# Kernel tuning notes

Hardware: AMD Instinct MI355X
Metric: run time of the kernel (lower is better)

## Reference

```python
import jax, jax.numpy as jnp
import numpy as np

N_NODES = 50000
N_EDGES = 800000
H = 64      # node_hidden_size
S = 16      # static_feature_size
EF = 16     # edge_feature_size
ATT_IN = 2 * H + 2 * S + EF   # 176
ATT_W = 2 * H + EF            # 144
UPD_IN = 2 * H                # 128
UPD_W = 2 * H                 # 128


def setup_inputs() -> dict:
    key = jax.random.key(0)
    ks = jax.random.split(key, 12)
    x = jax.random.normal(ks[0], (N_NODES, H), dtype=jnp.float32)
    x_s = jax.random.normal(ks[1], (N_NODES, S), dtype=jnp.float32)
    edge_index = jax.random.randint(ks[2], (2, N_EDGES), 0, N_NODES, dtype=jnp.int32)
    edge_features = jax.random.normal(ks[3], (N_EDGES, EF), dtype=jnp.float32)

    def lin(k, out_dim, in_dim):
        lim = 1.0 / np.sqrt(in_dim)
        kw, kb = jax.random.split(k)
        W = jax.random.uniform(kw, (out_dim, in_dim), minval=-lim, maxval=lim, dtype=jnp.float32)
        b = jax.random.uniform(kb, (out_dim,), minval=-lim, maxval=lim, dtype=jnp.float32)
        return W, b

    att_w1, att_b1 = lin(ks[4], ATT_W, ATT_IN)
    att_w2, att_b2 = lin(ks[5], 1, ATT_W)
    upd_w1, upd_b1 = lin(ks[6], UPD_W, UPD_IN)
    upd_w2, upd_b2 = lin(ks[7], H, UPD_W)

    return {
        "x": x, "x_s": x_s, "edge_index": edge_index, "edge_features": edge_features,
        "att_w1": att_w1, "att_b1": att_b1, "att_w2": att_w2, "att_b2": att_b2,
        "upd_w1": upd_w1, "upd_b1": upd_b1, "upd_w2": upd_w2, "upd_b2": upd_b2,
    }


def segment_softmax(scores, segment_ids, num_segments):
    max_scores = jax.ops.segment_max(scores, segment_ids, num_segments=num_segments)
    exp_scores = jnp.exp(scores - max_scores[segment_ids])
    sum_exp = jax.ops.segment_sum(exp_scores, segment_ids, num_segments=num_segments)
    return exp_scores / (sum_exp[segment_ids] + 1e-9)


def reference(x, x_s, edge_index, edge_features,
              att_w1, att_b1, att_w2, att_b2,
              upd_w1, upd_b1, upd_w2, upd_b2):
    num_nodes = x.shape[0]
    src, dst = edge_index[0], edge_index[1]

    # gather per-edge features: [E, 2H+2S+EF]
    att_in = jnp.concatenate(
        [x[src], x[dst], x_s[src], x_s[dst], edge_features], axis=-1)

    # attention MLP (depth=1, relu hidden), squeeze to [E]
    h = jax.nn.relu(att_in @ att_w1.T + att_b1)
    raw = (h @ att_w2.T + att_b2).squeeze(-1)
    raw = jax.nn.leaky_relu(raw)

    attn = segment_softmax(raw, dst, num_nodes)

    # weighted scatter-sum of source hidden feats -> [N, H]
    aggregated = jax.ops.segment_sum(x[src] * attn[:, None], dst, num_segments=num_nodes)

    upd_in = jnp.concatenate([x, aggregated], axis=-1)
    u = jax.nn.relu(upd_in @ upd_w1.T + upd_b1)
    out = u @ upd_w2.T + upd_b2
    return jax.nn.relu(out)
```

## Files before the change

### kernel.cpp

```cpp
#include <hip/hip_runtime.h>
#include <math.h>

#define N_NODES_C 50000
#define E_C       800000
#define ATT_IN_C  176
#define ATT_HID_C 144
#define SCAN_B    98
#define UPD_TILES 3125
#define DEG_B     3125
#define CVT_B     1978
#define SCORE_B   256

typedef __attribute__((ext_vector_type(8))) __bf16 bf16x8;
typedef __attribute__((ext_vector_type(4))) float f32x4;

#define O_RAW   0L
#define O_DEG   3200000L
#define O_OFF   3400704L
#define O_CUR   3601408L
#define O_CSR   3802112L
#define O_EFC   7002112L
#define O_XB    32602112L
#define O_XSB   39002112L
#define O_W1B   40602112L
#define O_UW1B  40653312L
#define O_UW2B  40686080L
#define O_AGGB  40702464L
#define O_PSUM  O_AGGB

__device__ __forceinline__ bf16x8 bzero8() {
    bf16x8 z;
#pragma unroll
    for (int i = 0; i < 8; ++i) z[i] = (__bf16)0.0f;
    return z;
}

__global__ __launch_bounds__(256) void k_prep(
    const int* __restrict__ ei,
    const float* __restrict__ x, const float* __restrict__ xs,
    const float* __restrict__ w1,
    const float* __restrict__ uw1, const float* __restrict__ uw2,
    int* __restrict__ deg,
    __bf16* __restrict__ xb, __bf16* __restrict__ xsb,
    __bf16* __restrict__ w1b,
    __bf16* __restrict__ uw1b, __bf16* __restrict__ uw2b)
{
    int bid = blockIdx.x;
    if (bid < DEG_B) {
        int e = bid * 256 + threadIdx.x;
        if (e < E_C) atomicAdd(&deg[ei[E_C + e]], 1);
        return;
    }
    long g = (long)(bid - DEG_B) * 256 + threadIdx.x;
    const long G_X = 400000, G_XS = 500000, G_W1 = 503168,
               G_UW1 = 505216, G_UW2 = 506240;
    if (g >= G_UW2) return;
    const float* src; __bf16* dst; long off;
    if (g < G_X)        { src = x;   dst = xb;   off = g * 8; }
    else if (g < G_XS)  { src = xs;  dst = xsb;  off = (g - G_X) * 8; }
    else if (g < G_W1)  { src = w1;  dst = w1b;  off = (g - G_XS) * 8; }
    else if (g < G_UW1) { src = uw1; dst = uw1b; off = (g - G_W1) * 8; }
    else                { src = uw2; dst = uw2b; off = (g - G_UW1) * 8; }
    float4 a = *(const float4*)(src + off);
    float4 b = *(const float4*)(src + off + 4);
    bf16x8 o;
    o[0] = (__bf16)a.x; o[1] = (__bf16)a.y; o[2] = (__bf16)a.z; o[3] = (__bf16)a.w;
    o[4] = (__bf16)b.x; o[5] = (__bf16)b.y; o[6] = (__bf16)b.z; o[7] = (__bf16)b.w;
    *(bf16x8*)(dst + off) = o;
}

__global__ __launch_bounds__(256) void k_scan1(const int* __restrict__ deg,
                                               int* __restrict__ psum) {
    __shared__ int red[256];
    int b = blockIdx.x, t = threadIdx.x;
    int i = b * 512 + t * 2;
    int s = 0;
    if (i < N_NODES_C) s += deg[i];
    if (i + 1 < N_NODES_C) s += deg[i + 1];
    red[t] = s;
    __syncthreads();
#pragma unroll
    for (int off = 128; off > 0; off >>= 1) {
        if (t < off) red[t] += red[t + off];
        __syncthreads();
    }
    if (t == 0) psum[b] = red[0];
}

__global__ __launch_bounds__(256) void k_scan3(const int* __restrict__ deg,
                                               const int* __restrict__ psum,
                                               int* __restrict__ offsets,
                                               int* __restrict__ cursor) {
    __shared__ int sc[256];
    __shared__ int bo[2];
    int b = blockIdx.x, t = threadIdx.x;
    if (t < 64) {
        int v1 = (t < SCAN_B) ? psum[t] : 0;
        int v2 = (t + 64 < SCAN_B) ? psum[t + 64] : 0;
        int c   = ((t < b) ? v1 : 0) + ((t + 64 < b) ? v2 : 0);
        int tot = v1 + v2;
#pragma unroll
        for (int off = 32; off > 0; off >>= 1) {
            c   += __shfl_xor(c, off, 64);
            tot += __shfl_xor(tot, off, 64);
        }
        if (t == 0) { bo[0] = c; bo[1] = tot; }
    }
    int i = b * 512 + t * 2;
    int d0 = (i < N_NODES_C) ? deg[i] : 0;
    int d1 = (i + 1 < N_NODES_C) ? deg[i + 1] : 0;
    int s = d0 + d1;
    sc[t] = s;
    __syncthreads();
#pragma unroll
    for (int off = 1; off < 256; off <<= 1) {
        int val = sc[t];
        int add = (t >= off) ? sc[t - off] : 0;
        __syncthreads();
        sc[t] = val + add;
        __syncthreads();
    }
    int excl = bo[0] + sc[t] - s;
    if (i < N_NODES_C)     { offsets[i]     = excl;      cursor[i]     = excl; }
    if (i + 1 < N_NODES_C) { offsets[i + 1] = excl + d0; cursor[i + 1] = excl + d0; }
    if (b == 0 && t == 0)  offsets[N_NODES_C] = bo[1];
}

__global__ __launch_bounds__(256) void k_fill(const int* __restrict__ ei,
                                              const float* __restrict__ ef,
                                              int* __restrict__ cursor,
                                              unsigned* __restrict__ csrp,
                                              __bf16* __restrict__ efc) {
    int e = blockIdx.x * blockDim.x + threadIdx.x;
    if (e < E_C) {
        int src  = ei[e];
        int dst  = ei[E_C + e];
        int slot = atomicAdd(&cursor[dst], 1);
        csrp[slot] = (unsigned)src | ((unsigned)dst << 16);
        const float4* efp = (const float4*)(ef + (long)e * 16);
        float4 f0 = efp[0], f1 = efp[1], f2 = efp[2], f3 = efp[3];
        bf16x8 o0, o1;
        o0[0] = (__bf16)f0.x; o0[1] = (__bf16)f0.y; o0[2] = (__bf16)f0.z; o0[3] = (__bf16)f0.w;
        o0[4] = (__bf16)f1.x; o0[5] = (__bf16)f1.y; o0[6] = (__bf16)f1.z; o0[7] = (__bf16)f1.w;
        o1[0] = (__bf16)f2.x; o1[1] = (__bf16)f2.y; o1[2] = (__bf16)f2.z; o1[3] = (__bf16)f2.w;
        o1[4] = (__bf16)f3.x; o1[5] = (__bf16)f3.y; o1[6] = (__bf16)f3.z; o1[7] = (__bf16)f3.w;
        __bf16* d = efc + (long)slot * 16;
        *(bf16x8*)d       = o0;
        *(bf16x8*)(d + 8) = o1;
    }
}

__device__ __forceinline__ void load_afrags(
    int src, int dst, long slot, int quad,
    const __bf16* __restrict__ xb, const __bf16* __restrict__ xsb,
    const __bf16* __restrict__ efc,
    bf16x8 a[6])
{
    const __bf16* px = xb + (long)src * 64 + quad * 8;
    const __bf16* pd = xb + (long)dst * 64 + quad * 8;
    a[0] = *(const bf16x8*)(px);
    a[1] = *(const bf16x8*)(px + 32);
    a[2] = *(const bf16x8*)(pd);
    a[3] = *(const bf16x8*)(pd + 32);
    if (quad < 2) {
        a[4] = *(const bf16x8*)(xsb + (long)src * 16 + quad * 8);
        a[5] = *(const bf16x8*)(efc + slot * 16 + quad * 8);
    } else {
        a[4] = *(const bf16x8*)(xsb + (long)dst * 16 + (quad - 2) * 8);
        a[5] = bzero8();
    }
}

__global__ __launch_bounds__(256) void k_scores_mfma(
    const __bf16* __restrict__ xb, const __bf16* __restrict__ xsb,
    const __bf16* __restrict__ efc, const __bf16* __restrict__ w1b,
    const unsigned* __restrict__ csrp,
    const float* __restrict__ b1, const float* __restrict__ w2,
    const float* __restrict__ b2, float* __restrict__ raw)
{
    __shared__ __bf16 w1s[144 * 184];
    int tid  = threadIdx.x;
    int lane = tid & 63;

    for (int c = tid; c < 144 * 22; c += 256) {
        int n = c / 22, kk = (c % 22) * 8;
        *(bf16x8*)&w1s[n * 184 + kk] = *(const bf16x8*)(w1b + (long)n * ATT_IN_C + kk);
    }
    for (int n = tid; n < 144; n += 256)
        *(bf16x8*)&w1s[n * 184 + 176] = bzero8();
    __syncthreads();

    int w = blockIdx.x * 4 + (tid >> 6);
    const int NP = E_C / 32;
    int per = (NP + 1023) / 1024;
    long j0 = (long)w * per;
    long j1 = j0 + per; if (j1 > NP) j1 = NP;
    if (j0 >= j1) return;

    int mrow = lane & 15;
    int quad = lane >> 4;
    const __bf16* wls = &w1s[mrow * 184 + quad * 8];

    float b1v[9], w2v[9];
#pragma unroll
    for (int nt = 0; nt < 9; ++nt) {
        int n = nt * 16 + mrow;
        b1v[nt] = b1[n];
        w2v[nt] = w2[n];
    }
    float b2v = b2[0];

    bf16x8 curA[6], curB[6], nxtA[6], nxtB[6];
    unsigned cA = 0, cB = 0;
    {
        unsigned e0 = csrp[j0 * 32 + mrow];
        unsigned e1 = csrp[j0 * 32 + 16 + mrow];
        load_afrags((int)(e0 & 0xFFFFu), (int)(e0 >> 16), j0 * 32 + mrow,
                    quad, xb, xsb, efc, curA);
        load_afrags((int)(e1 & 0xFFFFu), (int)(e1 >> 16), j0 * 32 + 16 + mrow,
                    quad, xb, xsb, efc, curB);
        if (j0 + 1 < j1) {
            unsigned f0 = csrp[(j0 + 1) * 32 + mrow];
            unsigned f1 = csrp[(j0 + 1) * 32 + 16 + mrow];
            load_afrags((int)(f0 & 0xFFFFu), (int)(f0 >> 16), (j0 + 1) * 32 + mrow,
                        quad, xb, xsb, efc, nxtA);
            load_afrags((int)(f1 & 0xFFFFu), (int)(f1 >> 16), (j0 + 1) * 32 + 16 + mrow,
                        quad, xb, xsb, efc, nxtB);
        }
    }

    for (long j = j0; j < j1; ++j) {
        if (j + 2 < j1) {
            cA = csrp[(j + 2) * 32 + mrow];
            cB = csrp[(j + 2) * 32 + 16 + mrow];
        }

        f32x4 accA[9], accB[9];
#pragma unroll
        for (int nt = 0; nt < 9; ++nt) {
            accA[nt] = (f32x4){0.f, 0.f, 0.f, 0.f};
            accB[nt] = (f32x4){0.f, 0.f, 0.f, 0.f};
        }

#pragma unroll
        for (int ks = 0; ks < 6; ++ks) {
#pragma unroll
            for (int nt = 0; nt < 9; ++nt) {
                bf16x8 bf = *(const bf16x8*)(wls + nt * (16 * 184) + ks * 32);
                accA[nt] = __builtin_amdgcn_mfma_f32_16x16x32_bf16(
                    curA[ks], bf, accA[nt], 0, 0, 0);
                accB[nt] = __builtin_amdgcn_mfma_f32_16x16x32_bf16(
                    curB[ks], bf, accB[nt], 0, 0, 0);
            }
        }

        float pA0 = 0.f, pA1 = 0.f, pA2 = 0.f, pA3 = 0.f;
        float pB0 = 0.f, pB1 = 0.f, pB2 = 0.f, pB3 = 0.f;
#pragma unroll
        for (int nt = 0; nt < 9; ++nt) {
            pA0 += w2v[nt] * fmaxf(accA[nt][0] + b1v[nt], 0.f);
            pA1 += w2v[nt] * fmaxf(accA[nt][1] + b1v[nt], 0.f);
            pA2 += w2v[nt] * fmaxf(accA[nt][2] + b1v[nt], 0.f);
            pA3 += w2v[nt] * fmaxf(accA[nt][3] + b1v[nt], 0.f);
            pB0 += w2v[nt] * fmaxf(accB[nt][0] + b1v[nt], 0.f);
            pB1 += w2v[nt] * fmaxf(accB[nt][1] + b1v[nt], 0.f);
            pB2 += w2v[nt] * fmaxf(accB[nt][2] + b1v[nt], 0.f);
            pB3 += w2v[nt] * fmaxf(accB[nt][3] + b1v[nt], 0.f);
        }
#pragma unroll
        for (int off = 1; off < 16; off <<= 1) {
            pA0 += __shfl_xor(pA0, off, 64);
            pA1 += __shfl_xor(pA1, off, 64);
            pA2 += __shfl_xor(pA2, off, 64);
            pA3 += __shfl_xor(pA3, off, 64);
            pB0 += __shfl_xor(pB0, off, 64);
            pB1 += __shfl_xor(pB1, off, 64);
            pB2 += __shfl_xor(pB2, off, 64);
            pB3 += __shfl_xor(pB3, off, 64);
        }
        if (mrow < 4) {
            float vA = (mrow == 0) ? pA0 : (mrow == 1) ? pA1 : (mrow == 2) ? pA2 : pA3;
            float vB = (mrow == 0) ? pB0 : (mrow == 1) ? pB1 : (mrow == 2) ? pB2 : pB3;
            vA += b2v; vB += b2v;
            vA = (vA >= 0.f) ? vA : 0.01f * vA;
            vB = (vB >= 0.f) ? vB : 0.01f * vB;
            raw[(j * 2) * 16 + quad * 4 + mrow]     = vA;
            raw[(j * 2 + 1) * 16 + quad * 4 + mrow] = vB;
        }

#pragma unroll
        for (int i = 0; i < 6; ++i) { curA[i] = nxtA[i]; curB[i] = nxtB[i]; }
        if (j + 2 < j1) {
            load_afrags((int)(cA & 0xFFFFu), (int)(cA >> 16), (j + 2) * 32 + mrow,
                        quad, xb, xsb, efc, nxtA);
            load_afrags((int)(cB & 0xFFFFu), (int)(cB >> 16), (j + 2) * 32 + 16 + mrow,
                        quad, xb, xsb, efc, nxtB);
        }
    }
}

__global__ __launch_bounds__(256) void k_agg(
    const __bf16* __restrict__ xb, const int* __restrict__ offsets,
    const unsigned* __restrict__ csrp,
    const float* __restrict__ raw, __bf16* __restrict__ aggb)
{
    int tid = threadIdx.x;
    int wave = tid >> 6, lane = tid & 63;
    int v = blockIdx.x * 4 + wave;
    if (v >= N_NODES_C) return;
    int s0 = offsets[v], s1 = offsets[v + 1];

    float m = -INFINITY;
    for (int p = s0 + lane; p < s1; p += 64) m = fmaxf(m, raw[p]);
#pragma unroll
    for (int off = 32; off > 0; off >>= 1) m = fmaxf(m, __shfl_xor(m, off, 64));

    float acc = 0.f, sum = 0.f;
    int p = s0;
    for (; p + 4 <= s1; p += 4) {
        unsigned c0 = csrp[p], c1 = csrp[p + 1], c2 = csrp[p + 2], c3 = csrp[p + 3];
        float r0 = raw[p], r1 = raw[p + 1], r2 = raw[p + 2], r3 = raw[p + 3];
        float v0 = (float)xb[(long)(c0 & 0xFFFFu) * 64 + lane];
        float v1 = (float)xb[(long)(c1 & 0xFFFFu) * 64 + lane];
        float v2 = (float)xb[(long)(c2 & 0xFFFFu) * 64 + lane];
        float v3 = (float)xb[(long)(c3 & 0xFFFFu) * 64 + lane];
        float w0 = expf(r0 - m), w1 = expf(r1 - m);
        float w2 = expf(r2 - m), w3 = expf(r3 - m);
        sum += (w0 + w1) + (w2 + w3);
        acc += w0 * v0 + w1 * v1 + w2 * v2 + w3 * v3;
    }
    for (; p < s1; ++p) {
        int src = (int)(csrp[p] & 0xFFFFu);
        float w = expf(raw[p] - m);
        sum += w;
        acc += w * (float)xb[(long)src * 64 + lane];
    }
    aggb[(long)v * 64 + lane] = (__bf16)(acc / (sum + 1e-9f));
}

__global__ __launch_bounds__(256) void k_upd_mfma(
    const __bf16* __restrict__ xb, const __bf16* __restrict__ aggb,
    const __bf16* __restrict__ w1b, const float* __restrict__ b1,
    const __bf16* __restrict__ w2b, const float* __restrict__ b2,
    float* __restrict__ out)
{
    __shared__ __bf16 ubuf[4][16 * 136];
    int tid = threadIdx.x, wid = tid >> 6, lane = tid & 63;
    int tile = blockIdx.x * 4 + wid;
    if (tile >= UPD_TILES) return;
    int mrow = lane & 15, quad = lane >> 4;

    long node = (long)tile * 16 + mrow;
    bf16x8 a1[4];
    a1[0] = *(const bf16x8*)(xb + node * 64 + quad * 8);
    a1[1] = *(const bf16x8*)(xb + node * 64 + 32 + quad * 8);
    a1[2] = *(const bf16x8*)(aggb + node * 64 + quad * 8);
    a1[3] = *(const bf16x8*)(aggb + node * 64 + 32 + quad * 8);

    bf16x8 b1f[4][8];
#pragma unroll
    for (int ks = 0; ks < 4; ++ks)
#pragma unroll
        for (int nt = 0; nt < 8; ++nt)
            b1f[ks][nt] = *(const bf16x8*)(w1b + (long)(nt * 16 + mrow) * 128 + ks * 32 + quad * 8);

    f32x4 acc1[8];
#pragma unroll
    for (int nt = 0; nt < 8; ++nt) acc1[nt] = (f32x4){0.f, 0.f, 0.f, 0.f};
#pragma unroll
    for (int ks = 0; ks < 4; ++ks)
#pragma unroll
        for (int nt = 0; nt < 8; ++nt)
            acc1[nt] = __builtin_amdgcn_mfma_f32_16x16x32_bf16(a1[ks], b1f[ks][nt], acc1[nt], 0, 0, 0);

    __bf16* ub = ubuf[wid];
#pragma unroll
    for (int nt = 0; nt < 8; ++nt) {
        float bb = b1[nt * 16 + mrow];
#pragma unroll
        for (int r = 0; r < 4; ++r) {
            float h = fmaxf(acc1[nt][r] + bb, 0.f);
            ub[(quad * 4 + r) * 136 + nt * 16 + mrow] = (__bf16)h;
        }
    }

    bf16x8 a2[4];
#pragma unroll
    for (int ks = 0; ks < 4; ++ks)
        a2[ks] = *(bf16x8*)&ub[mrow * 136 + ks * 32 + quad * 8];

    bf16x8 b2f[4][4];
#pragma unroll
    for (int ks = 0; ks < 4; ++ks)
#pragma unroll
        for (int nt = 0; nt < 4; ++nt)
            b2f[ks][nt] = *(const bf16x8*)(w2b + (long)(nt * 16 + mrow) * 128 + ks * 32 + quad * 8);

    f32x4 acc2[4];
#pragma unroll
    for (int nt = 0; nt < 4; ++nt) acc2[nt] = (f32x4){0.f, 0.f, 0.f, 0.f};
#pragma unroll
    for (int ks = 0; ks < 4; ++ks)
#pragma unroll
        for (int nt = 0; nt < 4; ++nt)
            acc2[nt] = __builtin_amdgcn_mfma_f32_16x16x32_bf16(a2[ks], b2f[ks][nt], acc2[nt], 0, 0, 0);

#pragma unroll
    for (int nt = 0; nt < 4; ++nt) {
        float bb = b2[nt * 16 + mrow];
#pragma unroll
        for (int r = 0; r < 4; ++r) {
            long nodeo = (long)tile * 16 + quad * 4 + r;
            out[nodeo * 64 + nt * 16 + mrow] = fmaxf(acc2[nt][r] + bb, 0.f);
        }
    }
}

extern "C" void kernel_launch(void* const* d_in, const int* in_sizes, int n_in,
                              void* d_out, int out_size, void* d_ws, size_t ws_size,
                              hipStream_t stream) {
    const float* x    = (const float*)d_in[0];
    const float* xs   = (const float*)d_in[1];
    const int*   ei   = (const int*)d_in[2];
    const float* ef   = (const float*)d_in[3];
    const float* aw1  = (const float*)d_in[4];
    const float* ab1  = (const float*)d_in[5];
    const float* aw2  = (const float*)d_in[6];
    const float* ab2  = (const float*)d_in[7];
    const float* uw1  = (const float*)d_in[8];
    const float* ub1  = (const float*)d_in[9];
    const float* uw2  = (const float*)d_in[10];
    const float* ub2  = (const float*)d_in[11];
    float* out = (float*)d_out;

    char* ws = (char*)d_ws;
    float*     raw     = (float*)(ws + O_RAW);
    int*       deg     = (int*)(ws + O_DEG);
    int*       offsets = (int*)(ws + O_OFF);
    int*       cursor  = (int*)(ws + O_CUR);
    unsigned*  csrp    = (unsigned*)(ws + O_CSR);
    __bf16*    efc     = (__bf16*)(ws + O_EFC);
    __bf16*    xb      = (__bf16*)(ws + O_XB);
    __bf16*    xsb     = (__bf16*)(ws + O_XSB);
    __bf16*    w1b     = (__bf16*)(ws + O_W1B);
    __bf16*    uw1b    = (__bf16*)(ws + O_UW1B);
    __bf16*    uw2b    = (__bf16*)(ws + O_UW2B);
    __bf16*    aggb    = (__bf16*)(ws + O_AGGB);
    int*       psum    = (int*)(ws + O_PSUM);

    hipMemsetAsync(deg, 0, N_NODES_C * sizeof(int), stream);
    hipLaunchKernelGGL(k_prep,     dim3(DEG_B + CVT_B),           dim3(256), 0, stream,
                       ei, x, xs, aw1, uw1, uw2, deg, xb, xsb, w1b, uw1b, uw2b);
    hipLaunchKernelGGL(k_scan1,    dim3(SCAN_B),                  dim3(256), 0, stream, deg, psum);
    hipLaunchKernelGGL(k_scan3,    dim3(SCAN_B),                  dim3(256), 0, stream,
                       deg, psum, offsets, cursor);
    hipLaunchKernelGGL(k_fill,     dim3((E_C + 255) / 256),       dim3(256), 0, stream,
                       ei, ef, cursor, csrp, efc);
    hipLaunchKernelGGL(k_scores_mfma, dim3(SCORE_B),              dim3(256), 0, stream,
                       xb, xsb, efc, w1b, csrp, ab1, aw2, ab2, raw);
    hipLaunchKernelGGL(k_agg,      dim3((N_NODES_C + 3) / 4),     dim3(256), 0, stream,
                       xb, offsets, csrp, raw, aggb);
    hipLaunchKernelGGL(k_upd_mfma, dim3((UPD_TILES + 3) / 4),     dim3(256), 0, stream,
                       xb, aggb, uw1b, ub1, uw2b, ub2, out);
}
```

Measured before the change: 348.9 us.

## Chunk attention MFMA accumulators and move bias/w2 to LDS to cut registers

The score kernel now computes the 144-wide hidden layer in three chunks of 48 columns, so only six accumulator tiles are live at once instead of eighteen. The per-lane b1/w2 register arrays move to shared memory, and the grid doubles from 256 to 512 blocks with work split across 2048 waves. The aim is lower VGPR pressure for higher occupancy and more waves to hide gather latency. The cost is extra LDS reads per chunk and shorter per-wave work, which may reduce prefetch pipelining benefit.

Measured after the change: 363.2 us. 1.04x slower.

```diff
diff --git a/kernel.cpp b/kernel.cpp
--- a/kernel.cpp
+++ b/kernel.cpp
@@ -9,7 +9,8 @@
 #define UPD_TILES 3125
 #define DEG_B     3125
 #define CVT_B     1978
-#define SCORE_B   256
+#define SCORE_B   512
+#define SCORE_WAVES (SCORE_B * 4)
 
 typedef __attribute__((ext_vector_type(8))) __bf16 bf16x8;
 typedef __attribute__((ext_vector_type(4))) float f32x4;
@@ -179,6 +180,8 @@
     const float* __restrict__ b2, float* __restrict__ raw)
 {
     __shared__ __bf16 w1s[144 * 184];
+    __shared__ float  b1s[144];
+    __shared__ float  w2s[144];
     int tid  = threadIdx.x;
     int lane = tid & 63;
 
@@ -186,13 +189,16 @@
         int n = c / 22, kk = (c % 22) * 8;
         *(bf16x8*)&w1s[n * 184 + kk] = *(const bf16x8*)(w1b + (long)n * ATT_IN_C + kk);
     }
-    for (int n = tid; n < 144; n += 256)
+    for (int n = tid; n < 144; n += 256) {
         *(bf16x8*)&w1s[n * 184 + 176] = bzero8();
+        b1s[n] = b1[n];
+        w2s[n] = w2[n];
+    }
     __syncthreads();
 
     int w = blockIdx.x * 4 + (tid >> 6);
     const int NP = E_C / 32;
-    int per = (NP + 1023) / 1024;
+    int per = (NP + SCORE_WAVES - 1) / SCORE_WAVES;
     long j0 = (long)w * per;
     long j1 = j0 + per; if (j1 > NP) j1 = NP;
     if (j0 >= j1) return;
@@ -200,14 +206,6 @@
     int mrow = lane & 15;
     int quad = lane >> 4;
     const __bf16* wls = &w1s[mrow * 184 + quad * 8];
-
-    float b1v[9], w2v[9];
-#pragma unroll
-    for (int nt = 0; nt < 9; ++nt) {
-        int n = nt * 16 + mrow;
-        b1v[nt] = b1[n];
-        w2v[nt] = w2[n];
-    }
     float b2v = b2[0];
 
     bf16x8 curA[6], curB[6], nxtA[6], nxtB[6];
@@ -235,38 +233,45 @@
             cB = csrp[(j + 2) * 32 + 16 + mrow];
         }
 
-        f32x4 accA[9], accB[9];
-#pragma unroll
-        for (int nt = 0; nt < 9; ++nt) {
-            accA[nt] = (f32x4){0.f, 0.f, 0.f, 0.f};
-            accB[nt] = (f32x4){0.f, 0.f, 0.f, 0.f};
-        }
-
-#pragma unroll
-        for (int ks = 0; ks < 6; ++ks) {
-#pragma unroll
-            for (int nt = 0; nt < 9; ++nt) {
-                bf16x8 bf = *(const bf16x8*)(wls + nt * (16 * 184) + ks * 32);
-                accA[nt] = __builtin_amdgcn_mfma_f32_16x16x32_bf16(
-                    curA[ks], bf, accA[nt], 0, 0, 0);
-                accB[nt] = __builtin_amdgcn_mfma_f32_16x16x32_bf16(
-                    curB[ks], bf, accB[nt], 0, 0, 0);
-            }
-        }
-
         float pA0 = 0.f, pA1 = 0.f, pA2 = 0.f, pA3 = 0.f;
         float pB0 = 0.f, pB1 = 0.f, pB2 = 0.f, pB3 = 0.f;
-#pragma unroll
-        for (int nt = 0; nt < 9; ++nt) {
-            pA0 += w2v[nt] * fmaxf(accA[nt][0] + b1v[nt], 0.f);
-            pA1 += w2v[nt] * fmaxf(accA[nt][1] + b1v[nt], 0.f);
-            pA2 += w2v[nt] * fmaxf(accA[nt][2] + b1v[nt], 0.f);
-            pA3 += w2v[nt] * fmaxf(accA[nt][3] + b1v[nt], 0.f);
-            pB0 += w2v[nt] * fmaxf(accB[nt][0] + b1v[nt], 0.f);
-            pB1 += w2v[nt] * fmaxf(accB[nt][1] + b1v[nt], 0.f);
-            pB2 += w2v[nt] * fmaxf(accB[nt][2] + b1v[nt], 0.f);
-            pB3 += w2v[nt] * fmaxf(accB[nt][3] + b1v[nt], 0.f);
-        }
+
+#pragma unroll
+        for (int ch = 0; ch < 3; ++ch) {
+            f32x4 aA[3], aB[3];
+#pragma unroll
+            for (int t = 0; t < 3; ++t) {
+                aA[t] = (f32x4){0.f, 0.f, 0.f, 0.f};
+                aB[t] = (f32x4){0.f, 0.f, 0.f, 0.f};
+            }
+#pragma unroll
+            for (int ks = 0; ks < 6; ++ks) {
+#pragma unroll
+                for (int t = 0; t < 3; ++t) {
+                    int nt = ch * 3 + t;
+                    bf16x8 bf = *(const bf16x8*)(wls + nt * (16 * 184) + ks * 32);
+                    aA[t] = __builtin_amdgcn_mfma_f32_16x16x32_bf16(
+                        curA[ks], bf, aA[t], 0, 0, 0);
+                    aB[t] = __builtin_amdgcn_mfma_f32_16x16x32_bf16(
+                        curB[ks], bf, aB[t], 0, 0, 0);
+                }
+            }
+#pragma unroll
+            for (int t = 0; t < 3; ++t) {
+                int nt = ch * 3 + t;
+                float bb = b1s[nt * 16 + mrow];
+                float ww = w2s[nt * 16 + mrow];
+                pA0 += ww * fmaxf(aA[t][0] + bb, 0.f);
+                pA1 += ww * fmaxf(aA[t][1] + bb, 0.f);
+                pA2 += ww * fmaxf(aA[t][2] + bb, 0.f);
+                pA3 += ww * fmaxf(aA[t][3] + bb, 0.f);
+                pB0 += ww * fmaxf(aB[t][0] + bb, 0.f);
+                pB1 += ww * fmaxf(aB[t][1] + bb, 0.f);
+                pB2 += ww * fmaxf(aB[t][2] + bb, 0.f);
+                pB3 += ww * fmaxf(aB[t][3] + bb, 0.f);
+            }
+        }
+
 #pragma unroll
         for (int off = 1; off < 16; off <<= 1) {
             pA0 += __shfl_xor(pA0, off, 64);
```
